# Kernel optimization log

Measured on AMD Instinct MI355X. Metric: run time of the kernel, lower is better.

Reference implementation:

```python
import math
import jax, jax.numpy as jnp
import numpy as np

B, D, E, R, TOP_K = 16384, 2048, 64, 128, 2
TAU = 1.0
CAP_FACTOR = 1.25
TOP_C = min(E, max(4, 2 * TOP_K))  # GatingNetwork default top_c


def setup_inputs() -> dict:
    key = jax.random.key(0)
    ks = jax.random.split(key, 7)
    x = jax.random.normal(ks[0], (B, D), dtype=jnp.float32)
    # shared_encoder: nn.Linear(d, d) -> weight [out, in], bias [out]
    We = jax.random.normal(ks[1], (D, D), dtype=jnp.float32) / np.sqrt(D)
    be = jnp.zeros((D,), dtype=jnp.float32)
    # gating: nn.Linear(d, E, bias=False) -> weight [E, d]
    Wg = jax.random.normal(ks[2], (E, D), dtype=jnp.float32) / np.sqrt(D)
    # LowRankExpert per expert: U [r, d], V [d, r], gamma scalar (init 1.0)
    U = jax.random.normal(ks[3], (E, R, D), dtype=jnp.float32) / np.sqrt(D)
    V = jax.random.normal(ks[4], (E, D, R), dtype=jnp.float32) / np.sqrt(R)
    gamma = jnp.ones((E,), dtype=jnp.float32)
    return {"x": x, "We": We, "be": be, "Wg": Wg, "U": U, "V": V, "gamma": gamma}


def reference(x, We, be, Wg, U, V, gamma):
    # shared encoder
    enc = x @ We.T + be  # [B, D]

    # ---- gating: top-C candidates then top-K routing ----
    logits = (enc @ Wg.T) / TAU  # [B, E]
    topc_vals, topc_idx = jax.lax.top_k(logits, TOP_C)          # [B, C]
    topk_vals, pos_in_c = jax.lax.top_k(topc_vals, TOP_K)       # [B, K]
    topk_idx = jnp.take_along_axis(topc_idx, pos_in_c, axis=1)  # [B, K]
    # masked stable softmax over the K selected logits (with 1e-12 eps as in source)
    m = jnp.max(topk_vals, axis=-1, keepdims=True)
    ex = jnp.exp(topk_vals - m)
    w = ex / (jnp.sum(ex, axis=-1, keepdims=True) + 1e-12)      # [B, K]

    # ---- flatten assignments ----
    N = B * TOP_K
    tok = jnp.repeat(jnp.arange(B), TOP_K)   # [N]
    eid = topk_idx.reshape(-1)               # [N]
    wf = w.reshape(-1)                       # [N]
    wmask = wf > 1e-12

    # ---- capacity-based dispatch (sort/group equivalent, fixed shapes) ----
    cap = int(math.ceil(CAP_FACTOR * N / E))  # expert capacity
    onehot = ((eid[:, None] == jnp.arange(E)[None, :]) & wmask[:, None]).astype(jnp.int32)  # [N, E]
    pos = jnp.cumsum(onehot, axis=0) - onehot                      # position within expert
    pos_of = jnp.take_along_axis(pos, eid[:, None], axis=1)[:, 0]  # [N]
    valid = wmask & (pos_of < cap)
    slot = jnp.where(valid, pos_of, cap)  # overflow -> dummy slot (never occurs at this cap)

    # gather tokens to per-expert buffers [E, cap+1, D]
    xbuf = jnp.zeros((E, cap + 1, D), dtype=enc.dtype).at[eid, slot].set(enc[tok])

    # batched low-rank experts: delta = gamma * V @ silu(U @ x)
    h = jax.nn.silu(jnp.einsum('ecd,erd->ecr', xbuf, U))
    delta = jnp.einsum('ecr,edr->ecd', h, V) * gamma[:, None, None]  # [E, cap+1, D]

    # scatter-combine: y = enc + sum_k w_k * delta_k (residual handled since sum w = 1)
    dflat = delta[eid, slot]  # [N, D]
    y = enc.at[tok].add(jnp.where(valid, wf, 0.0)[:, None] * dflat)
    return y
```

## Files before the change

kernel.cpp:

```cpp
#include <hip/hip_runtime.h>
#include <math.h>

#define NTOK 16384
#define DDIM 2048
#define NEXP 64
#define RRANK 128
#define CAP 640

typedef __attribute__((ext_vector_type(8))) short bf16x8;
typedef __attribute__((ext_vector_type(4))) float f32x4;
typedef __attribute__((address_space(1))) const unsigned int gu32_t;
typedef __attribute__((address_space(3))) unsigned int lu32_t;

__device__ __forceinline__ void gload16(const void* g, void* l) {
  __builtin_amdgcn_global_load_lds((gu32_t*)g, (lu32_t*)l, 16, 0, 0);
}

__device__ __forceinline__ float silu_f(float v) {
  return v / (1.f + expf(-v));
}

__device__ __forceinline__ unsigned short f2bf(float f) {
  unsigned int u = __float_as_uint(f);
  unsigned int r = (u + 0x7fffu + ((u >> 16) & 1u)) >> 16;
  return (unsigned short)r;
}

__device__ __forceinline__ float bf2f(unsigned short u) {
  return __uint_as_float(((unsigned int)u) << 16);
}

__device__ __forceinline__ int swz256(int d) {
  return d ^ (((d >> 8) & 7) << 4);
}

__global__ __launch_bounds__(256) void cvt_all_kernel(
    const float* __restrict__ x, const float* __restrict__ We,
    const float* __restrict__ U, const float* __restrict__ V,
    unsigned short* __restrict__ xb, unsigned short* __restrict__ Web,
    unsigned short* __restrict__ Ub, unsigned short* __restrict__ Vb)
{
  const int S0 = NTOK * DDIM / 4;
  const int S1 = DDIM * DDIM / 4;
  const int S2 = NEXP * RRANK * DDIM / 4;
  const int total = S0 + S1 + 2 * S2;
  int i = blockIdx.x * 256 + threadIdx.x;
  const int stride = gridDim.x * 256;
  for (; i < total; i += stride) {
    const float* in; unsigned short* out; int j;
    if (i < S0) { in = x; out = xb; j = i; }
    else if (i < S0 + S1) { in = We; out = Web; j = i - S0; }
    else if (i < S0 + S1 + S2) { in = U; out = Ub; j = i - S0 - S1; }
    else { in = V; out = Vb; j = i - S0 - S1 - S2; }
    const float4 v = ((const float4*)in)[j];
    ushort4 o;
    o.x = f2bf(v.x); o.y = f2bf(v.y); o.z = f2bf(v.z); o.w = f2bf(v.w);
    ((ushort4*)out)[j] = o;
  }
}

__global__ __launch_bounds__(512, 2) void enc_mfma5(
    const unsigned short* __restrict__ xb, const unsigned short* __restrict__ Web,
    const float* __restrict__ be, unsigned short* __restrict__ encbf)
{
  __shared__ unsigned short LDS[65536];
  const int tid = threadIdx.x;
  const int lane = tid & 63, wid = tid >> 6;
  const int wr = wid >> 2, wc = wid & 3;
  const int fr = lane & 15, fq = lane >> 4;
  const int bid = blockIdx.x;
  const int wg = (bid & 7) * 64 + (bid >> 3);
  const int n0 = (wg & 7) * 256, m0 = (wg >> 3) * 256;

  const unsigned short* asb[4];
  const unsigned short* bsb[4];
  int d4[4];
#pragma unroll
  for (int is = 0; is < 4; ++is) {
    const int doff = is * 8192 + tid * 16;
    const int r = doff >> 7;
    const int cs = ((doff >> 4) & 7) ^ (r & 7);
    asb[is] = xb + (size_t)(m0 + r) * DDIM + cs * 8;
    bsb[is] = Web + (size_t)(n0 + r) * DDIM + cs * 8;
    d4[is] = doff;
  }

  auto STAGE = [&](int buf, int kb) {
#pragma unroll
    for (int is = 0; is < 4; ++is) {
      gload16(asb[is] + kb, (char*)(LDS + buf * 16384) + d4[is]);
      gload16(bsb[is] + kb, (char*)(LDS + 32768 + buf * 16384) + d4[is]);
    }
  };

  f32x4 acc[8][4];
#pragma unroll
  for (int m = 0; m < 8; ++m)
#pragma unroll
    for (int n = 0; n < 4; ++n) acc[m][n] = (f32x4){0.f, 0.f, 0.f, 0.f};

  STAGE(0, 0);
  STAGE(1, 64);
  asm volatile("s_waitcnt vmcnt(8)" ::: "memory");
  __builtin_amdgcn_s_barrier();
  asm volatile("" ::: "memory");

#pragma unroll 1
  for (int t = 0; t < 32; ++t) {
    const int cur = t & 1;
    const unsigned short* Ab = LDS + cur * 16384;
    const unsigned short* Bb = LDS + 32768 + cur * 16384;

    bf16x8 bfv[4][2];
#pragma unroll
    for (int n = 0; n < 4; ++n) {
      const int row = wc * 64 + n * 16 + fr;
#pragma unroll
      for (int kk = 0; kk < 2; ++kk)
        bfv[n][kk] = *(const bf16x8*)((const char*)Bb +
                      row * 128 + (((kk * 4 + fq) ^ (row & 7)) << 4));
    }
#pragma unroll
    for (int mh = 0; mh < 2; ++mh) {
      bf16x8 af[4][2];
#pragma unroll
      for (int m = 0; m < 4; ++m) {
        const int row = wr * 128 + (mh * 4 + m) * 16 + fr;
#pragma unroll
        for (int kk = 0; kk < 2; ++kk)
          af[m][kk] = *(const bf16x8*)((const char*)Ab +
                       row * 128 + (((kk * 4 + fq) ^ (row & 7)) << 4));
      }
      __builtin_amdgcn_s_setprio(1);
#pragma unroll
      for (int m = 0; m < 4; ++m)
#pragma unroll
        for (int n = 0; n < 4; ++n)
#pragma unroll
          for (int kk = 0; kk < 2; ++kk)
            acc[mh * 4 + m][n] = __builtin_amdgcn_mfma_f32_16x16x32_bf16(
                af[m][kk], bfv[n][kk], acc[mh * 4 + m][n], 0, 0, 0);
      __builtin_amdgcn_s_setprio(0);
    }

    asm volatile("" ::: "memory");
    __builtin_amdgcn_s_barrier();
    if (t < 30) {
      STAGE(cur, (t + 2) * 64);
      asm volatile("s_waitcnt vmcnt(8)" ::: "memory");
    } else {
      asm volatile("s_waitcnt vmcnt(0)" ::: "memory");
    }
    __builtin_amdgcn_s_barrier();
    asm volatile("" ::: "memory");
  }

  float bias[4];
#pragma unroll
  for (int n = 0; n < 4; ++n) bias[n] = be[n0 + wc * 64 + n * 16 + fr];
#pragma unroll
  for (int m = 0; m < 8; ++m) {
#pragma unroll
    for (int j = 0; j < 4; ++j) {
      const int row = m0 + wr * 128 + m * 16 + fq * 4 + j;
      unsigned short* ob = encbf + (size_t)row * DDIM + n0 + wc * 64 + fr;
#pragma unroll
      for (int n = 0; n < 4; ++n)
        ob[n * 16] = f2bf(acc[m][n][j] + bias[n]);
    }
  }
}

__global__ __launch_bounds__(256) void gmat_part_kernel(
    const float* __restrict__ We, const float* __restrict__ Wg,
    double* __restrict__ Gpart)
{
  __shared__ float As[64][68];
  __shared__ float Bs[64][68];
  const int tid = threadIdx.x;
  const int d0 = blockIdx.x * 64;
  const int oc = blockIdx.y;
  const int tx = tid & 15, ty = tid >> 4;
  const int row = tid >> 2, p = (tid & 3) * 16;

  double acc[4][4];
#pragma unroll
  for (int j = 0; j < 4; ++j)
#pragma unroll
    for (int i = 0; i < 4; ++i) acc[j][i] = 0.0;

  for (int o0 = oc * 256; o0 < oc * 256 + 256; o0 += 64) {
    float4 wv[4], gv[4];
#pragma unroll
    for (int q = 0; q < 4; ++q) {
      wv[q] = *(const float4*)(We + (size_t)(o0 + row) * DDIM + d0 + p + q * 4);
      gv[q] = *(const float4*)(Wg + (size_t)row * DDIM + o0 + p + q * 4);
    }
    __syncthreads();
#pragma unroll
    for (int q = 0; q < 4; ++q) {
      const int c = p + q * 4;
      As[row][c + 0] = wv[q].x; As[row][c + 1] = wv[q].y;
      As[row][c + 2] = wv[q].z; As[row][c + 3] = wv[q].w;
      Bs[c + 0][row] = gv[q].x; Bs[c + 1][row] = gv[q].y;
      Bs[c + 2][row] = gv[q].z; Bs[c + 3][row] = gv[q].w;
    }
    __syncthreads();
#pragma unroll 8
    for (int oo = 0; oo < 64; ++oo) {
      double a[4], b[4];
#pragma unroll
      for (int j = 0; j < 4; ++j) a[j] = (double)As[oo][ty * 4 + j];
#pragma unroll
      for (int i = 0; i < 4; ++i) b[i] = (double)Bs[oo][tx * 4 + i];
#pragma unroll
      for (int j = 0; j < 4; ++j)
#pragma unroll
        for (int i = 0; i < 4; ++i)
          acc[j][i] = fma(a[j], b[i], acc[j][i]);
    }
    __syncthreads();
  }
#pragma unroll
  for (int j = 0; j < 4; ++j)
#pragma unroll
    for (int i = 0; i < 4; ++i) {
      const int d = d0 + ty * 4 + j, e = tx * 4 + i;
      Gpart[(size_t)oc * (DDIM * NEXP) + (size_t)e * DDIM + d] = acc[j][i];
    }
}

__global__ __launch_bounds__(256) void greduce_kernel(
    const double* __restrict__ Gpart, double* __restrict__ Gt,
    unsigned short* __restrict__ Gbf)
{
  const int idx = blockIdx.x * 256 + threadIdx.x;
  double s = 0.0;
#pragma unroll
  for (int oc = 0; oc < 8; ++oc)
    s += Gpart[(size_t)oc * (DDIM * NEXP) + idx];
  Gt[idx] = s;
  Gbf[idx] = f2bf((float)s);
}

__global__ __launch_bounds__(256) void bias_c_kernel(
    const float* __restrict__ be, const float* __restrict__ Wg,
    double* __restrict__ c64)
{
  const int e = blockIdx.x;
  const int tid = threadIdx.x;
  double s = 0.0;
  for (int o = tid; o < DDIM; o += 256)
    s += (double)be[o] * (double)Wg[(size_t)e * DDIM + o];
  __shared__ double red[256];
  red[tid] = s;
  __syncthreads();
  for (int st = 128; st > 0; st >>= 1) {
    if (tid < st) red[tid] += red[tid + st];
    __syncthreads();
  }
  if (tid == 0) c64[e] = red[0];
}

__global__ __launch_bounds__(256) void logits_topc_kernel(
    const unsigned short* __restrict__ xb, const unsigned short* __restrict__ Gbf,
    const double* __restrict__ c64, int* __restrict__ cand8)
{
  __shared__ unsigned short At[128 * 32];
  __shared__ unsigned short Bt[64 * 32];
  __shared__ float Ls[128][64];
  const int tid = threadIdx.x;
  const int lane = tid & 63, wid = tid >> 6;
  const int fr = lane & 15, fq = lane >> 4;
  const int t0 = blockIdx.x * 128;

  const int doff0 = wid * 1024 + lane * 16;
  const int doff1 = doff0 + 4096;
  const unsigned short* as0 = xb + (size_t)(t0 + (doff0 >> 6)) * DDIM + ((doff0 & 63) >> 1);
  const unsigned short* as1 = xb + (size_t)(t0 + (doff1 >> 6)) * DDIM + ((doff1 & 63) >> 1);
  const unsigned short* bs0 = Gbf + (size_t)(doff0 >> 6) * DDIM + ((doff0 & 63) >> 1);
  char* ad0 = (char*)At + doff0; char* ad1 = (char*)At + doff1;
  char* bd0 = (char*)Bt + doff0;

  f32x4 acc[2][4];
#pragma unroll
  for (int m = 0; m < 2; ++m)
#pragma unroll
    for (int n = 0; n < 4; ++n) acc[m][n] = (f32x4){0.f, 0.f, 0.f, 0.f};

  for (int kb = 0; kb < DDIM; kb += 32) {
    __syncthreads();
    gload16(as0 + kb, ad0);
    gload16(as1 + kb, ad1);
    gload16(bs0 + kb, bd0);
    __syncthreads();
    bf16x8 af[2], bfr[4];
#pragma unroll
    for (int m = 0; m < 2; ++m)
      af[m] = *(const bf16x8*)&At[(wid * 32 + m * 16 + fr) * 32 + fq * 8];
#pragma unroll
    for (int n = 0; n < 4; ++n)
      bfr[n] = *(const bf16x8*)&Bt[(n * 16 + fr) * 32 + fq * 8];
#pragma unroll
    for (int m = 0; m < 2; ++m)
#pragma unroll
      for (int n = 0; n < 4; ++n)
        acc[m][n] = __builtin_amdgcn_mfma_f32_16x16x32_bf16(af[m], bfr[n], acc[m][n], 0, 0, 0);
  }

#pragma unroll
  for (int m = 0; m < 2; ++m)
#pragma unroll
    for (int j = 0; j < 4; ++j) {
      const int row = wid * 32 + m * 16 + fq * 4 + j;
#pragma unroll
      for (int n = 0; n < 4; ++n)
        Ls[row][n * 16 + fr] = acc[m][n][j];
    }
  __syncthreads();

  if (tid < 128) {
    float v8[8];
    int i8[8];
#pragma unroll
    for (int c = 0; c < 8; ++c) { v8[c] = -INFINITY; i8[c] = 0; }
    for (int e = 0; e < NEXP; ++e) {
      const float v = Ls[tid][e] + (float)c64[e];
      if (v > v8[7]) {
        int p = 7;
        while (p > 0 && v > v8[p - 1]) { v8[p] = v8[p - 1]; i8[p] = i8[p - 1]; --p; }
        v8[p] = v; i8[p] = e;
      }
    }
    int* cp = cand8 + (size_t)(t0 + tid) * 8;
#pragma unroll
    for (int c = 0; c < 8; ++c) cp[c] = i8[c];
  }
}

__global__ __launch_bounds__(256) void refine_kernel(
    const float* __restrict__ x, const double* __restrict__ Gt,
    const double* __restrict__ c64, const int* __restrict__ cand8,
    int* __restrict__ topk, float* __restrict__ wkf)
{
  const int t = blockIdx.x;
  const int tid = threadIdx.x;
  const int lane = tid & 63, w = tid >> 6;
  __shared__ float xs[DDIM];
  __shared__ double red[8][4];

  ((float4*)xs)[tid] = ((const float4*)(x + (size_t)t * DDIM))[tid];
  ((float4*)xs)[tid + 256] = ((const float4*)(x + (size_t)t * DDIM))[tid + 256];
  __syncthreads();

  int myc[8];
#pragma unroll
  for (int c = 0; c < 8; ++c) myc[c] = cand8[(size_t)t * 8 + c];

#pragma unroll
  for (int c = 0; c < 8; ++c) {
    const double* g = Gt + (size_t)myc[c] * DDIM;
    double s = 0.0;
#pragma unroll
    for (int q = 0; q < 8; ++q) {
      const int d = q * 256 + tid;
      s += (double)xs[d] * g[d];
    }
#pragma unroll
    for (int off = 32; off > 0; off >>= 1) s += __shfl_down(s, off);
    if (lane == 0) red[c][w] = s;
  }
  __syncthreads();

  if (tid == 0) {
    double v1 = -1e300, v2 = -1e300;
    int i1 = 0, i2 = 0;
#pragma unroll
    for (int c = 0; c < 8; ++c) {
      const double v = red[c][0] + red[c][1] + red[c][2] + red[c][3] + c64[myc[c]];
      if (v > v1) { v2 = v1; i2 = i1; v1 = v; i1 = myc[c]; }
      else if (v > v2) { v2 = v; i2 = myc[c]; }
    }
    const double e2 = exp(v2 - v1);
    const double s = 1.0 + e2 + 1e-12;
    topk[2 * t] = i1; topk[2 * t + 1] = i2;
    wkf[2 * t] = (float)(1.0 / s);
    wkf[2 * t + 1] = (float)(e2 / s);
  }
}

__global__ __launch_bounds__(256) void route_kernel(
    const int* __restrict__ topk, const float* __restrict__ wkf,
    int* __restrict__ slots , int* __restrict__ counts_eff,
    int* __restrict__ val )
{
  const int e = blockIdx.x;
  const int tid = threadIdx.x;
  const int lane = tid & 63, wave = tid >> 6;
  const int base0 = wave * 8192;
  __shared__ int wcnt[4];

  int cnt = 0;
  for (int c = 0; c < 8192; c += 64) {
    const int a = base0 + c + lane;
    const bool match = (topk[a] == e) && (wkf[a] > 1e-12f);
    cnt += (int)__popcll(__ballot(match));
  }
  if (lane == 0) wcnt[wave] = cnt;
  __syncthreads();

  int run = 0;
  for (int w = 0; w < 4; ++w)
    if (w < wave) run += wcnt[w];
  const int total = wcnt[0] + wcnt[1] + wcnt[2] + wcnt[3];

  for (int c = 0; c < 8192; c += 64) {
    const int a = base0 + c + lane;
    const bool match = (topk[a] == e) && (wkf[a] > 1e-12f);
    const unsigned long long bal = __ballot(match);
    const int rank = run + (int)__popcll(bal & ((1ull << lane) - 1ull));
    if (match && rank < CAP) {
      slots[e * CAP + rank] = a;
      val[a] = 1;
    }
    run += (int)__popcll(bal);
  }
  if (tid == 0) counts_eff[e] = (total < CAP) ? total : CAP;
}

__global__ __launch_bounds__(256) void expert_fused(
    const unsigned short* __restrict__ encbf, const unsigned short* __restrict__ Ub,
    const unsigned short* __restrict__ Vb, const float* __restrict__ gamma,
    const int* __restrict__ counts_eff, const int* __restrict__ slots,
    const float* __restrict__ wkf, unsigned short* __restrict__ Dbuf)
{
  const int lin = blockIdx.x;
  const int wg = (lin & 7) * 80 + (lin >> 3);
  const int e = wg / 10;
  const int t0 = (wg % 10) * 64;
  const int cnt = counts_eff[e];
  if (t0 >= cnt) return;

  __shared__ int aid[64];
  __shared__ int toks[64];
  __shared__ float wts[64];
  __shared__ unsigned short Ht[64 * 128];
  __shared__ char U2[32768];

  const int tid = threadIdx.x;
  const int lane = tid & 63, wid = tid >> 6;
  const int wr = wid >> 1, wc = wid & 1;
  const int fr = lane & 15, fq = lane >> 4;

  if (tid < 64) {
    const int i = t0 + tid;
    if (i < cnt) {
      const int a = slots[e * CAP + i];
      aid[tid] = a;
      toks[tid] = a >> 1;
      wts[tid] = wkf[a] * gamma[e];
    } else {
      aid[tid] = -1;
      toks[tid] = slots[e * CAP] >> 1;
      wts[tid] = 0.f;
    }
  }
  __syncthreads();

  unsigned short* At = (unsigned short*)U2;
  unsigned short* Bt = (unsigned short*)(U2 + 8192);
  const unsigned short* Ue = Ub + (size_t)e * RRANK * DDIM;

  size_t aoff[2]; char* adst[2];
#pragma unroll
  for (int is = 0; is < 2; ++is) {
    const int doff = is * 4096 + tid * 16;
    const int r = doff >> 7;
    const int cs = ((doff >> 4) & 7) ^ (r & 7);
    aoff[is] = (size_t)toks[r] * DDIM + cs * 8;
    adst[is] = (char*)At + doff;
  }
  const unsigned short* bsrc[4]; char* bdst[4];
#pragma unroll
  for (int is = 0; is < 4; ++is) {
    const int doff = is * 4096 + tid * 16;
    const int r = doff >> 7;
    const int cs = ((doff >> 4) & 7) ^ (r & 7);
    bsrc[is] = Ue + (size_t)r * DDIM + cs * 8;
    bdst[is] = (char*)Bt + doff;
  }

  f32x4 hacc[2][4];
#pragma unroll
  for (int m = 0; m < 2; ++m)
#pragma unroll
    for (int n = 0; n < 4; ++n) hacc[m][n] = (f32x4){0.f, 0.f, 0.f, 0.f};

  for (int kb = 0; kb < DDIM; kb += 64) {
    __syncthreads();
    gload16(encbf + aoff[0] + kb, adst[0]);
    gload16(encbf + aoff[1] + kb, adst[1]);
#pragma unroll
    for (int is = 0; is < 4; ++is)
      gload16(bsrc[is] + kb, bdst[is]);
    __syncthreads();
#pragma unroll
    for (int kk = 0; kk < 2; ++kk) {
      bf16x8 af[2], bfv[4];
#pragma unroll
      for (int m = 0; m < 2; ++m) {
        const int row = wr * 32 + m * 16 + fr;
        af[m] = *(const bf16x8*)((const char*)At +
                 row * 128 + (((kk * 4 + fq) ^ (row & 7)) << 4));
      }
#pragma unroll
      for (int n = 0; n < 4; ++n) {
        const int row = wc * 64 + n * 16 + fr;
        bfv[n] = *(const bf16x8*)((const char*)Bt +
                  row * 128 + (((kk * 4 + fq) ^ (row & 7)) << 4));
      }
#pragma unroll
      for (int m = 0; m < 2; ++m)
#pragma unroll
        for (int n = 0; n < 4; ++n)
          hacc[m][n] = __builtin_amdgcn_mfma_f32_16x16x32_bf16(af[m], bfv[n], hacc[m][n], 0, 0, 0);
    }
  }

  __syncthreads();
#pragma unroll
  for (int m = 0; m < 2; ++m) {
#pragma unroll
    for (int j = 0; j < 4; ++j) {
      const int row = wr * 32 + m * 16 + fq * 4 + j;
#pragma unroll
      for (int n = 0; n < 4; ++n) {
        const int col = wc * 64 + n * 16 + fr;
        const int b = (row * 256 + col * 2) ^ ((row & 7) << 4);
        *(unsigned short*)((char*)Ht + b) = f2bf(silu_f(hacc[m][n][j]));
      }
    }
  }
  __syncthreads();

  unsigned short* Vt = (unsigned short*)U2;
  const unsigned short* Ve = Vb + (size_t)e * DDIM * RRANK;
  const int hd = tid * 16;

  bf16x8 paf[2][4];
  float wv[2][4];
  int av[2][4];
#pragma unroll
  for (int m = 0; m < 2; ++m) {
    const int row = wr * 32 + m * 16 + fr;
#pragma unroll
    for (int kk = 0; kk < 4; ++kk) {
      const int b = (row * 256 + kk * 64 + fq * 16) ^ ((row & 7) << 4);
      paf[m][kk] = *(const bf16x8*)((const char*)Ht + b);
    }
#pragma unroll
    for (int j = 0; j < 4; ++j) {
      const int tl = wr * 32 + m * 16 + fq * 4 + j;
      wv[m][j] = wts[tl];
      av[m][j] = aid[tl];
    }
  }

  for (int nb = 0; nb < 16; ++nb) {
    __syncthreads();
    const unsigned short* vsrc = Ve + (size_t)nb * 128 * RRANK;
#pragma unroll
    for (int is = 0; is < 8; ++is) {
      const int d = is * 4096 + hd;
      gload16(vsrc + (swz256(d) >> 1), (char*)Vt + d);
    }
    __syncthreads();

    f32x4 acc[2][4];
#pragma unroll
    for (int m = 0; m < 2; ++m)
#pragma unroll
      for (int n = 0; n < 4; ++n) acc[m][n] = (f32x4){0.f, 0.f, 0.f, 0.f};

#pragma unroll
    for (int n = 0; n < 4; ++n) {
      const int drow = wc * 64 + n * 16 + fr;
#pragma unroll
      for (int kk = 0; kk < 4; ++kk) {
        const int b = (drow * 256 + kk * 64 + fq * 16) ^ ((drow & 7) << 4);
        const bf16x8 bfr = *(const bf16x8*)((const char*)Vt + b);
#pragma unroll
        for (int m = 0; m < 2; ++m)
          acc[m][n] = __builtin_amdgcn_mfma_f32_16x16x32_bf16(paf[m][kk], bfr, acc[m][n], 0, 0, 0);
      }
    }

#pragma unroll
    for (int m = 0; m < 2; ++m) {
#pragma unroll
      for (int j = 0; j < 4; ++j) {
        if (av[m][j] >= 0) {
          const float w = wv[m][j];
          unsigned short* dp = Dbuf + (size_t)av[m][j] * DDIM + nb * 128 + wc * 64 + fr;
#pragma unroll
          for (int n = 0; n < 4; ++n)
            dp[n * 16] = f2bf(acc[m][n][j] * w);
        }
      }
    }
  }
}

__global__ __launch_bounds__(256) void combine_kernel(
    const unsigned short* __restrict__ encbf, const unsigned short* __restrict__ Dbuf,
    const int* __restrict__ val, float* __restrict__ y)
{
  const int t = blockIdx.x;
  const int tid = threadIdx.x;
  const int c0 = tid * 8;
  float* yp = y + (size_t)t * DDIM + c0;
  const int v0 = val[2 * t], v1 = val[2 * t + 1];

  const ushort4 e0 = *(const ushort4*)(encbf + (size_t)t * DDIM + c0);
  const ushort4 e1 = *(const ushort4*)(encbf + (size_t)t * DDIM + c0 + 4);
  float o[8] = {bf2f(e0.x), bf2f(e0.y), bf2f(e0.z), bf2f(e0.w),
                bf2f(e1.x), bf2f(e1.y), bf2f(e1.z), bf2f(e1.w)};

  if (v0) {
    const ushort4 d0 = *(const ushort4*)(Dbuf + (size_t)(2 * t) * DDIM + c0);
    const ushort4 d1 = *(const ushort4*)(Dbuf + (size_t)(2 * t) * DDIM + c0 + 4);
    o[0] += bf2f(d0.x); o[1] += bf2f(d0.y); o[2] += bf2f(d0.z); o[3] += bf2f(d0.w);
    o[4] += bf2f(d1.x); o[5] += bf2f(d1.y); o[6] += bf2f(d1.z); o[7] += bf2f(d1.w);
  }
  if (v1) {
    const ushort4 d0 = *(const ushort4*)(Dbuf + (size_t)(2 * t + 1) * DDIM + c0);
    const ushort4 d1 = *(const ushort4*)(Dbuf + (size_t)(2 * t + 1) * DDIM + c0 + 4);
    o[0] += bf2f(d0.x); o[1] += bf2f(d0.y); o[2] += bf2f(d0.z); o[3] += bf2f(d0.w);
    o[4] += bf2f(d1.x); o[5] += bf2f(d1.y); o[6] += bf2f(d1.z); o[7] += bf2f(d1.w);
  }
  *(float4*)(yp) = (float4){o[0], o[1], o[2], o[3]};
  *(float4*)(yp + 4) = (float4){o[4], o[5], o[6], o[7]};
}

extern "C" void kernel_launch(void* const* d_in, const int* in_sizes, int n_in,
                              void* d_out, int out_size, void* d_ws, size_t ws_size,
                              hipStream_t stream)
{
  const float* x     = (const float*)d_in[0];
  const float* We    = (const float*)d_in[1];
  const float* be    = (const float*)d_in[2];
  const float* Wg    = (const float*)d_in[3];
  const float* U     = (const float*)d_in[4];
  const float* V     = (const float*)d_in[5];
  const float* gamma = (const float*)d_in[6];
  float* y = (float*)d_out;

  char* ws = (char*)d_ws;
  int*            topk       = (int*)(ws + 0);
  float*          wkf        = (float*)(ws + 131072);
  int*            counts_eff = (int*)(ws + 262144);
  double*         c64        = (double*)(ws + 262400);
  int*            cand8      = (int*)(ws + 262912);
  double*         Gt         = (double*)(ws + 787200);
  unsigned short* G_bf       = (unsigned short*)(ws + 1835776);
  int*            slots      = (int*)(ws + 2097920);
  int*            val        = (int*)(ws + 2261760);
  unsigned short* Dbuf       = (unsigned short*)(ws + 2392832);
  unsigned short* x_bf       = (unsigned short*)(ws + 2392832);
  unsigned short* We_bf      = (unsigned short*)(ws + 69501696);
  double*         Gpart      = (double*)(ws + 77890304);
  unsigned short* U_bf       = (unsigned short*)(ws + 136610560);
  unsigned short* V_bf       = (unsigned short*)(ws + 170164992);
  unsigned short* enc_bf     = (unsigned short*)(ws + 203719424);

  hipMemsetAsync(val, 0, 131072, stream);

  cvt_all_kernel<<<dim3(2048), 256, 0, stream>>>(x, We, U, V, x_bf, We_bf, U_bf, V_bf);

  gmat_part_kernel<<<dim3(32, 8), 256, 0, stream>>>(We, Wg, Gpart);
  greduce_kernel<<<dim3(512), 256, 0, stream>>>(Gpart, Gt, G_bf);
  bias_c_kernel<<<dim3(64), 256, 0, stream>>>(be, Wg, c64);
  logits_topc_kernel<<<dim3(128), 256, 0, stream>>>(x_bf, G_bf, c64, cand8);
  refine_kernel<<<dim3(NTOK), 256, 0, stream>>>(x, Gt, c64, cand8, topk, wkf);
  route_kernel<<<dim3(64), 256, 0, stream>>>(topk, wkf, slots, counts_eff, val);

  enc_mfma5<<<dim3(512), 512, 0, stream>>>(x_bf, We_bf, be, enc_bf);
  expert_fused<<<dim3(640), 256, 0, stream>>>(enc_bf, U_bf, V_bf, gamma, counts_eff, slots, wkf, Dbuf);
  combine_kernel<<<dim3(NTOK), 256, 0, stream>>>(enc_bf, Dbuf, val, y);
}
```

Baseline: 702.5 us.

## Double-buffer V tiles in expert up-projection with async prefetch

The expert V-projection loop now splits the output dimension into 64-column tiles that alternate between two LDS buffers. The next tile is prefetched with global_load_lds while the current one is consumed, and hand-placed s_waitcnt vmcnt plus barriers replace the two full __syncthreads per iteration. The first two tiles are issued before the H-silu write so their load latency overlaps that work, and s_setprio raises wave priority around the MFMA block. The trade-offs are more loop iterations with smaller tiles and fragile manual counter-based synchronisation. The vmcnt(4) waits also count the interleaved Dbuf global stores, so the assumed number of outstanding loads may not hold.

```diff
diff --git a/kernel.cpp b/kernel.cpp
--- a/kernel.cpp
+++ b/kernel.cpp
@@ -526,8 +526,21 @@
           hacc[m][n] = __builtin_amdgcn_mfma_f32_16x16x32_bf16(af[m], bfv[n], hacc[m][n], 0, 0, 0);
     }
   }
-
   __syncthreads();
+
+  const unsigned short* Ve = Vb + (size_t)e * DDIM * RRANK;
+  auto STAGEV = [&](int buf, int nh) {
+    const unsigned short* vs = Ve + (size_t)nh * 64 * RRANK;
+    char* vd = U2 + buf * 16384;
+#pragma unroll
+    for (int is = 0; is < 4; ++is) {
+      const int d = is * 4096 + tid * 16;
+      gload16(vs + (swz256(d) >> 1), vd + d);
+    }
+  };
+  STAGEV(0, 0);
+  STAGEV(1, 1);
+
 #pragma unroll
   for (int m = 0; m < 2; ++m) {
 #pragma unroll
@@ -541,11 +554,9 @@
       }
     }
   }
-  __syncthreads();
-
-  unsigned short* Vt = (unsigned short*)U2;
-  const unsigned short* Ve = Vb + (size_t)e * DDIM * RRANK;
-  const int hd = tid * 16;
+  asm volatile("s_waitcnt lgkmcnt(0)" ::: "memory");
+  __builtin_amdgcn_s_barrier();
+  asm volatile("" ::: "memory");
 
   bf16x8 paf[2][4];
   float wv[2][4];
@@ -566,34 +577,34 @@
     }
   }
 
-  for (int nb = 0; nb < 16; ++nb) {
-    __syncthreads();
-    const unsigned short* vsrc = Ve + (size_t)nb * 128 * RRANK;
-#pragma unroll
-    for (int is = 0; is < 8; ++is) {
-      const int d = is * 4096 + hd;
-      gload16(vsrc + (swz256(d) >> 1), (char*)Vt + d);
-    }
-    __syncthreads();
-
-    f32x4 acc[2][4];
+  asm volatile("s_waitcnt vmcnt(4)" ::: "memory");
+  __builtin_amdgcn_s_barrier();
+  asm volatile("" ::: "memory");
+
+#pragma unroll 1
+  for (int h = 0; h < 32; ++h) {
+    const char* Vh = U2 + (h & 1) * 16384;
+
+    f32x4 acc[2][2];
 #pragma unroll
     for (int m = 0; m < 2; ++m)
 #pragma unroll
-      for (int n = 0; n < 4; ++n) acc[m][n] = (f32x4){0.f, 0.f, 0.f, 0.f};
-
-#pragma unroll
-    for (int n = 0; n < 4; ++n) {
-      const int drow = wc * 64 + n * 16 + fr;
+      for (int n = 0; n < 2; ++n) acc[m][n] = (f32x4){0.f, 0.f, 0.f, 0.f};
+
+    __builtin_amdgcn_s_setprio(1);
+#pragma unroll
+    for (int n = 0; n < 2; ++n) {
+      const int drl = wc * 32 + n * 16 + fr;
 #pragma unroll
       for (int kk = 0; kk < 4; ++kk) {
-        const int b = (drow * 256 + kk * 64 + fq * 16) ^ ((drow & 7) << 4);
-        const bf16x8 bfr = *(const bf16x8*)((const char*)Vt + b);
+        const int b = (drl * 256 + kk * 64 + fq * 16) ^ ((drl & 7) << 4);
+        const bf16x8 bfr = *(const bf16x8*)(Vh + b);
 #pragma unroll
         for (int m = 0; m < 2; ++m)
           acc[m][n] = __builtin_amdgcn_mfma_f32_16x16x32_bf16(paf[m][kk], bfr, acc[m][n], 0, 0, 0);
       }
     }
+    __builtin_amdgcn_s_setprio(0);
 
 #pragma unroll
     for (int m = 0; m < 2; ++m) {
@@ -601,13 +612,23 @@
       for (int j = 0; j < 4; ++j) {
         if (av[m][j] >= 0) {
           const float w = wv[m][j];
-          unsigned short* dp = Dbuf + (size_t)av[m][j] * DDIM + nb * 128 + wc * 64 + fr;
-#pragma unroll
-          for (int n = 0; n < 4; ++n)
-            dp[n * 16] = f2bf(acc[m][n][j] * w);
+          unsigned short* dp = Dbuf + (size_t)av[m][j] * DDIM + h * 64 + wc * 32 + fr;
+          dp[0]  = f2bf(acc[m][0][j] * w);
+          dp[16] = f2bf(acc[m][1][j] * w);
         }
       }
     }
+
+    asm volatile("" ::: "memory");
+    __builtin_amdgcn_s_barrier();
+    if (h < 30) {
+      STAGEV(h & 1, h + 2);
+      asm volatile("s_waitcnt vmcnt(4)" ::: "memory");
+    } else {
+      asm volatile("s_waitcnt vmcnt(0)" ::: "memory");
+    }
+    __builtin_amdgcn_s_barrier();
+    asm volatile("" ::: "memory");
   }
 }
 
```

Result: no change. 708.1 us (+0.8%).
